# Optimization experiments

Hardware: AMD Instinct MI355X
Metric: run time of the kernel (lower is better)

Reference implementation:

```python
import jax, jax.numpy as jnp
import numpy as np

N_NODES = 100000
N_EDGES = 1600000
D_IN = 64
D_OUT = 64
NEG_SLOPE = 0.2


def setup_inputs() -> dict:
    key = jax.random.key(0)
    ks = jax.random.split(key, 10)
    x = jax.random.normal(ks[0], (N_NODES, D_IN), dtype=jnp.float32)
    edge_index = jax.random.randint(ks[1], (2, N_EDGES), 0, N_NODES, dtype=jnp.int64)
    # glorot-ish scales
    s_lin = 1.0 / np.sqrt(D_IN)
    W_lin = jax.random.normal(ks[2], (D_IN, D_OUT), dtype=jnp.float32) * s_lin
    att_src = jax.random.normal(ks[3], (D_OUT,), dtype=jnp.float32) * s_lin
    att_dst = jax.random.normal(ks[4], (D_OUT,), dtype=jnp.float32) * s_lin
    bias = jnp.zeros((D_OUT,), dtype=jnp.float32)
    W1 = jax.random.normal(ks[5], (D_IN, D_OUT // 2), dtype=jnp.float32) * s_lin
    b1 = jnp.zeros((D_OUT // 2,), dtype=jnp.float32)
    W2 = jax.random.normal(ks[6], (D_OUT // 2, 1), dtype=jnp.float32) * (1.0 / np.sqrt(D_OUT // 2))
    b2 = jnp.zeros((1,), dtype=jnp.float32)
    return {"x": x, "edge_index": edge_index, "W_lin": W_lin, "att_src": att_src,
            "att_dst": att_dst, "bias": bias, "W1": W1, "b1": b1, "W2": W2, "b2": b2}


def reference(x, edge_index, W_lin, att_src, att_dst, bias, W1, b1, W2, b2):
    N = x.shape[0]
    h = x @ W_lin  # [N, D_OUT]
    # peak detector applied to projected features (module requires in==out)
    peak = jax.nn.sigmoid(jax.nn.gelu(h @ W1 + b1, approximate=False) @ W2 + b2)  # [N,1]
    row, col = edge_index[0], edge_index[1]
    # (cat(src,dst) * att).sum(-1) == (h@att_src)[row] + (h@att_dst)[col]
    a_s = h @ att_src  # [N]
    a_d = h @ att_dst  # [N]
    alpha = a_s[row] + a_d[col]  # [E]
    alpha = jnp.where(alpha >= 0, alpha, NEG_SLOPE * alpha)  # leaky_relu
    # segment softmax keyed on row
    m = jax.ops.segment_max(alpha, row, num_segments=N)  # [N]
    e = jnp.exp(alpha - m[row])
    s = jax.ops.segment_sum(e, row, num_segments=N)  # [N]
    alpha = e / s[row]
    # scatter-add weighted source messages back to row (dropout=identity in eval)
    out = jax.ops.segment_sum(h[row] * alpha[:, None], row, num_segments=N)  # [N, D_OUT]
    out = out * (1.0 + peak) + bias
    return out
```

## Files before the change

kernel.cpp:

```cpp
#include <hip/hip_runtime.h>
#include <math.h>

#define D 64
#define DH 32

typedef __attribute__((ext_vector_type(8))) short bf16x8;
typedef __attribute__((ext_vector_type(4))) float f32x4;

static __device__ __forceinline__ unsigned short f2b(float f) {
    unsigned int u = __builtin_bit_cast(unsigned int, f);
    u += 0x7FFFu + ((u >> 16) & 1u);
    return (unsigned short)(u >> 16);
}
static __device__ __forceinline__ unsigned int pack_b2(float a, float b) {
    return (unsigned int)f2b(a) | ((unsigned int)f2b(b) << 16);
}
static __device__ __forceinline__ float gelu_exact(float v) {
    return 0.5f * v * (1.0f + erff(v * 0.70710678118654752f));
}

__global__ void edge_flag_kernel(const int* __restrict__ row,
                                 unsigned char* __restrict__ flag, int E) {
    int i4 = (blockIdx.x * blockDim.x + threadIdx.x) * 4;
    if (i4 + 3 < E) {
        int4 r = *(const int4*)(row + i4);
        flag[r.x] = 1; flag[r.y] = 1; flag[r.z] = 1; flag[r.w] = 1;
    } else if (i4 < E) {
        for (int j = i4; j < E; ++j) flag[row[j]] = 1;
    }
}

__global__ void prep_kernel(const float* __restrict__ Wlin, const float* __restrict__ W1,
                            const float* __restrict__ bias, const float* __restrict__ b1,
                            const float* __restrict__ W2,
                            uint4* __restrict__ flag4, int nflag4,
                            unsigned short* __restrict__ packAW,
                            unsigned short* __restrict__ packAW1, float* __restrict__ packBias,
                            float* __restrict__ packB1, float* __restrict__ packW2)
{
    const int idx = blockIdx.x * blockDim.x + threadIdx.x;
    const int stride = gridDim.x * blockDim.x;
    const uint4 z = {0u, 0u, 0u, 0u};
    for (int i = idx; i < nflag4; i += stride) flag4[i] = z;

    if (blockIdx.x == 0) {
        const int lane = threadIdx.x & 63, part = threadIdx.x >> 6;
        const int q = lane >> 4, m = lane & 15;
#pragma unroll
        for (int fo = 0; fo < 2; ++fo) {
            const int f = part * 2 + fo, nt = f >> 1, ks = f & 1;
#pragma unroll
            for (int j = 0; j < 8; ++j) {
                const int k = 32 * ks + 8 * q + j, n = 16 * nt + m;
                packAW[(f * 64 + lane) * 8 + j] = f2b(Wlin[k * D + n]);
            }
        }
        {
            const int f = part, ntW = f >> 1, ks = f & 1;
#pragma unroll
            for (int j = 0; j < 8; ++j) {
                const int k = 32 * ks + 8 * q + j, n = 16 * ntW + m;
                packAW1[(f * 64 + lane) * 8 + j] = f2b(W1[k * DH + n]);
            }
        }
#pragma unroll
        for (int r = 0; r < 4; ++r)
            packBias[(part * 64 + lane) * 4 + r] = bias[16 * part + 4 * q + r];
        if (part < 2) {
#pragma unroll
            for (int r = 0; r < 4; ++r)
                packB1[(part * 64 + lane) * 4 + r] = b1[16 * part + 4 * q + r];
        } else {
#pragma unroll
            for (int r = 0; r < 4; ++r)
                packW2[((part - 2) * 64 + lane) * 4 + r] = W2[16 * (part - 2) + 4 * q + r];
        }
    }
}

__global__ __launch_bounds__(128) void gat_mfma3(
    const float* __restrict__ x, const unsigned char* __restrict__ flag,
    const unsigned short* __restrict__ packAW, const unsigned short* __restrict__ packAW1,
    const float* __restrict__ packBias, const float* __restrict__ packB1,
    const float* __restrict__ packW2, const float* __restrict__ b2,
    float* __restrict__ out, int N)
{
    __shared__ unsigned short sH[2][64][72];

    const int tid  = threadIdx.x;
    const int wv   = tid >> 6;
    const int lane = tid & 63;
    const int q    = lane >> 4;
    const int m    = lane & 15;
    const int nodeBase = blockIdx.x * 128 + wv * 64;

    int gn[4]; unsigned char fl[4];
#pragma unroll
    for (int mt = 0; mt < 4; ++mt) {
        int g = nodeBase + 16 * mt + m;
        if (g > N - 1) g = N - 1;
        gn[mt] = g;
        fl[mt] = flag[g];
    }
    const float b2s = b2[0];

    float4 u[4][4];
#pragma unroll
    for (int mt = 0; mt < 4; ++mt) {
        const float* px = x + (size_t)gn[mt] * D + 8 * q;
#pragma unroll
        for (int ks = 0; ks < 2; ++ks) {
            u[mt][2 * ks + 0] = *(const float4*)(px + 32 * ks);
            u[mt][2 * ks + 1] = *(const float4*)(px + 32 * ks + 4);
        }
    }

    bf16x8 aw[4][2];
#pragma unroll
    for (int nt = 0; nt < 4; ++nt)
#pragma unroll
        for (int ks = 0; ks < 2; ++ks)
            aw[nt][ks] = ((const bf16x8*)packAW)[(nt * 2 + ks) * 64 + lane];

    bf16x8 bx[4][2];
#pragma unroll
    for (int mt = 0; mt < 4; ++mt)
#pragma unroll
        for (int ks = 0; ks < 2; ++ks) {
            const float4 u0 = u[mt][2 * ks + 0], u1 = u[mt][2 * ks + 1];
            uint4 pk;
            pk.x = pack_b2(u0.x, u0.y); pk.y = pack_b2(u0.z, u0.w);
            pk.z = pack_b2(u1.x, u1.y); pk.w = pack_b2(u1.z, u1.w);
            bx[mt][ks] = __builtin_bit_cast(bf16x8, pk);
        }

    f32x4 accH[4][4];
#pragma unroll
    for (int mt = 0; mt < 4; ++mt)
#pragma unroll
        for (int nt = 0; nt < 4; ++nt)
            accH[mt][nt] = (f32x4){0.f, 0.f, 0.f, 0.f};
#pragma unroll
    for (int ks = 0; ks < 2; ++ks)
#pragma unroll
        for (int mt = 0; mt < 4; ++mt)
#pragma unroll
            for (int nt = 0; nt < 4; ++nt)
                accH[mt][nt] = __builtin_amdgcn_mfma_f32_16x16x32_bf16(
                    aw[nt][ks], bx[mt][ks], accH[mt][nt], 0, 0, 0);

#pragma unroll
    for (int mt = 0; mt < 4; ++mt)
#pragma unroll
        for (int nt = 0; nt < 4; ++nt) {
            uint2 pk;
            pk.x = pack_b2(accH[mt][nt][0], accH[mt][nt][1]);
            pk.y = pack_b2(accH[mt][nt][2], accH[mt][nt][3]);
            *(uint2*)&sH[wv][16 * mt + m][16 * nt + 4 * q] = pk;
        }
    bf16x8 a2[4][2];
#pragma unroll
    for (int mt = 0; mt < 4; ++mt)
#pragma unroll
        for (int ks = 0; ks < 2; ++ks)
            a2[mt][ks] = *(const bf16x8*)&sH[wv][16 * mt + m][32 * ks + 8 * q];

    bf16x8 aw1[2][2];
#pragma unroll
    for (int nt = 0; nt < 2; ++nt)
#pragma unroll
        for (int ks = 0; ks < 2; ++ks)
            aw1[nt][ks] = ((const bf16x8*)packAW1)[(nt * 2 + ks) * 64 + lane];
    const f32x4 b1v0 = ((const f32x4*)packB1)[0 * 64 + lane];
    const f32x4 b1v1 = ((const f32x4*)packB1)[1 * 64 + lane];
    f32x4 acc2[2][4];
#pragma unroll
    for (int mt = 0; mt < 4; ++mt) { acc2[0][mt] = b1v0; acc2[1][mt] = b1v1; }
#pragma unroll
    for (int ks = 0; ks < 2; ++ks)
#pragma unroll
        for (int nt = 0; nt < 2; ++nt)
#pragma unroll
            for (int mt = 0; mt < 4; ++mt)
                acc2[nt][mt] = __builtin_amdgcn_mfma_f32_16x16x32_bf16(
                    aw1[nt][ks], a2[mt][ks], acc2[nt][mt], 0, 0, 0);

    const f32x4 w2v0 = ((const f32x4*)packW2)[0 * 64 + lane];
    const f32x4 w2v1 = ((const f32x4*)packW2)[1 * 64 + lane];
    float scale[4];
#pragma unroll
    for (int mt = 0; mt < 4; ++mt) {
        float pp = 0.f;
#pragma unroll
        for (int r = 0; r < 4; ++r) {
            pp = fmaf(gelu_exact(acc2[0][mt][r]), w2v0[r], pp);
            pp = fmaf(gelu_exact(acc2[1][mt][r]), w2v1[r], pp);
        }
        pp += __shfl_xor(pp, 16);
        pp += __shfl_xor(pp, 32);
        scale[mt] = (fl[mt] != 0) ? (1.f + 1.f / (1.f + expf(-(pp + b2s)))) : 0.f;
    }

    f32x4 biasv[4];
#pragma unroll
    for (int nt = 0; nt < 4; ++nt) biasv[nt] = ((const f32x4*)packBias)[nt * 64 + lane];
#pragma unroll
    for (int mt = 0; mt < 4; ++mt) {
        const int g = nodeBase + 16 * mt + m;
        if (g < N) {
            float* po = out + (size_t)g * D + 4 * q;
#pragma unroll
            for (int nt = 0; nt < 4; ++nt) {
                f32x4 o;
#pragma unroll
                for (int r = 0; r < 4; ++r)
                    o[r] = fmaf(accH[mt][nt][r], scale[mt], biasv[nt][r]);
                *(f32x4*)(po + 16 * nt) = o;
            }
        }
    }
}

extern "C" void kernel_launch(void* const* d_in, const int* in_sizes, int n_in,
                              void* d_out, int out_size, void* d_ws, size_t ws_size,
                              hipStream_t stream) {
    const float* x    = (const float*)d_in[0];
    const int*   eidx = (const int*)d_in[1];
    const float* Wlin = (const float*)d_in[2];
    const float* bias = (const float*)d_in[5];
    const float* W1   = (const float*)d_in[6];
    const float* b1   = (const float*)d_in[7];
    const float* W2   = (const float*)d_in[8];
    const float* b2   = (const float*)d_in[9];
    float* out = (float*)d_out;

    const int N = in_sizes[0] / D;
    const int E = in_sizes[1] / 2;

    char* ws = (char*)d_ws;
    unsigned char* flag = (unsigned char*)ws;
    const int nflag4 = (N + 15) / 16;
    const size_t off = (((size_t)nflag4 * 16) + 255) & ~(size_t)255;
    unsigned short* packAW  = (unsigned short*)(ws + off);
    unsigned short* packAW1 = (unsigned short*)(ws + off + 8192);
    float*          packBias= (float*)(ws + off + 12288);
    float*          packB1  = (float*)(ws + off + 16384);
    float*          packW2  = (float*)(ws + off + 18432);

    prep_kernel<<<128, 256, 0, stream>>>(Wlin, W1, bias, b1, W2,
                                         (uint4*)flag, nflag4,
                                         packAW, packAW1, packBias, packB1, packW2);
    edge_flag_kernel<<<(E / 4 + 255) / 256, 256, 0, stream>>>(eidx, flag, E);
    gat_mfma3<<<(N + 127) / 128, 128, 0, stream>>>(x, flag, packAW, packAW1,
                                                   packBias, packB1, packW2, b2, out, N);
}
```

Baseline: 36.20 us.

## Stage x tiles and packed weights into LDS via direct global-to-LDS loads

The main kernel now gives each wave 32 nodes instead of 64 and uses 256-thread blocks. It loads x rows and all packed weights and biases straight into LDS with global_load_lds, using an XOR swizzle so the later reads avoid bank conflicts, then reuses the same LDS region for the bf16 hidden staging. The edge-flag kernel now reads each flag and only writes it when it is still unset, cutting redundant byte stores. The cost is a block-wide barrier and 52KB of LDS per block, which may limit occupancy.

```diff
diff --git a/kernel.cpp b/kernel.cpp
--- a/kernel.cpp
+++ b/kernel.cpp
@@ -17,6 +17,11 @@
 }
 static __device__ __forceinline__ float gelu_exact(float v) {
     return 0.5f * v * (1.0f + erff(v * 0.70710678118654752f));
+}
+static __device__ __forceinline__ void gload_lds16(void* l, const void* g) {
+    __builtin_amdgcn_global_load_lds(
+        (const __attribute__((address_space(1))) unsigned int*)g,
+        (__attribute__((address_space(3))) unsigned int*)l, 16, 0, 0);
 }
 
 __global__ void edge_flag_kernel(const int* __restrict__ row,
@@ -24,7 +29,10 @@
     int i4 = (blockIdx.x * blockDim.x + threadIdx.x) * 4;
     if (i4 + 3 < E) {
         int4 r = *(const int4*)(row + i4);
-        flag[r.x] = 1; flag[r.y] = 1; flag[r.z] = 1; flag[r.w] = 1;
+        if (!flag[r.x]) flag[r.x] = 1;
+        if (!flag[r.y]) flag[r.y] = 1;
+        if (!flag[r.z]) flag[r.z] = 1;
+        if (!flag[r.w]) flag[r.w] = 1;
     } else if (i4 < E) {
         for (int j = i4; j < E; ++j) flag[row[j]] = 1;
     }
@@ -78,118 +86,129 @@
     }
 }
 
-__global__ __launch_bounds__(128) void gat_mfma3(
+__global__ __launch_bounds__(256) void gat_mfma4(
     const float* __restrict__ x, const unsigned char* __restrict__ flag,
-    const unsigned short* __restrict__ packAW, const unsigned short* __restrict__ packAW1,
-    const float* __restrict__ packBias, const float* __restrict__ packB1,
-    const float* __restrict__ packW2, const float* __restrict__ b2,
+    const float* __restrict__ packbuf, const float* __restrict__ b2,
     float* __restrict__ out, int N)
 {
-    __shared__ unsigned short sH[2][64][72];
+    __shared__ unsigned char lds[53248];
 
     const int tid  = threadIdx.x;
     const int wv   = tid >> 6;
     const int lane = tid & 63;
     const int q    = lane >> 4;
     const int m    = lane & 15;
-    const int nodeBase = blockIdx.x * 128 + wv * 64;
-
-    int gn[4]; unsigned char fl[4];
-#pragma unroll
-    for (int mt = 0; mt < 4; ++mt) {
+    const int nodeBase = blockIdx.x * 128 + wv * 32;
+    const int XB = wv * 8192;
+
+    unsigned char fl[2];
+#pragma unroll
+    for (int mt = 0; mt < 2; ++mt) {
         int g = nodeBase + 16 * mt + m;
         if (g > N - 1) g = N - 1;
-        gn[mt] = g;
         fl[mt] = flag[g];
     }
     const float b2s = b2[0];
 
-    float4 u[4][4];
-#pragma unroll
-    for (int mt = 0; mt < 4; ++mt) {
-        const float* px = x + (size_t)gn[mt] * D + 8 * q;
+#pragma unroll
+    for (int j = 0; j < 8; ++j) {
+        const int r_loc = j * 4 + (lane >> 4);
+        int grow = nodeBase + r_loc;
+        if (grow > N - 1) grow = N - 1;
+        const int c = lane & 15;
+        const float* src = x + (size_t)grow * D + ((c ^ (r_loc & 7)) * 4);
+        gload_lds16(lds + XB + j * 1024, src);
+    }
+#pragma unroll
+    for (int i = 0; i < 5; ++i) {
+        const int ch = wv * 5 + i;
+        gload_lds16(lds + 32768 + ch * 1024, packbuf + ch * 256 + lane * 4);
+    }
+    __syncthreads();
+
+    bf16x8 aw[4][2];
+#pragma unroll
+    for (int nt = 0; nt < 4; ++nt)
+#pragma unroll
+        for (int ks = 0; ks < 2; ++ks)
+            aw[nt][ks] = *(const bf16x8*)(lds + 32768 + (nt * 2 + ks) * 1024 + lane * 16);
+
+    bf16x8 bx[2][2];
+#pragma unroll
+    for (int mt = 0; mt < 2; ++mt) {
+        const int r = 16 * mt + m;
 #pragma unroll
         for (int ks = 0; ks < 2; ++ks) {
-            u[mt][2 * ks + 0] = *(const float4*)(px + 32 * ks);
-            u[mt][2 * ks + 1] = *(const float4*)(px + 32 * ks + 4);
-        }
-    }
-
-    bf16x8 aw[4][2];
-#pragma unroll
-    for (int nt = 0; nt < 4; ++nt)
-#pragma unroll
-        for (int ks = 0; ks < 2; ++ks)
-            aw[nt][ks] = ((const bf16x8*)packAW)[(nt * 2 + ks) * 64 + lane];
-
-    bf16x8 bx[4][2];
-#pragma unroll
-    for (int mt = 0; mt < 4; ++mt)
-#pragma unroll
-        for (int ks = 0; ks < 2; ++ks) {
-            const float4 u0 = u[mt][2 * ks + 0], u1 = u[mt][2 * ks + 1];
+            const int c0 = ks * 8 + q * 2;
+            const uint4 lo = *(const uint4*)(lds + XB + r * 256 + ((c0 ^ (r & 7)) * 16));
+            const uint4 hi = *(const uint4*)(lds + XB + r * 256 + (((c0 + 1) ^ (r & 7)) * 16));
+            const float4 u0 = __builtin_bit_cast(float4, lo);
+            const float4 u1 = __builtin_bit_cast(float4, hi);
             uint4 pk;
             pk.x = pack_b2(u0.x, u0.y); pk.y = pack_b2(u0.z, u0.w);
             pk.z = pack_b2(u1.x, u1.y); pk.w = pack_b2(u1.z, u1.w);
             bx[mt][ks] = __builtin_bit_cast(bf16x8, pk);
         }
-
-    f32x4 accH[4][4];
-#pragma unroll
-    for (int mt = 0; mt < 4; ++mt)
+    }
+
+    f32x4 accH[2][4];
+#pragma unroll
+    for (int mt = 0; mt < 2; ++mt)
 #pragma unroll
         for (int nt = 0; nt < 4; ++nt)
             accH[mt][nt] = (f32x4){0.f, 0.f, 0.f, 0.f};
 #pragma unroll
     for (int ks = 0; ks < 2; ++ks)
 #pragma unroll
-        for (int mt = 0; mt < 4; ++mt)
+        for (int mt = 0; mt < 2; ++mt)
 #pragma unroll
             for (int nt = 0; nt < 4; ++nt)
                 accH[mt][nt] = __builtin_amdgcn_mfma_f32_16x16x32_bf16(
                     aw[nt][ks], bx[mt][ks], accH[mt][nt], 0, 0, 0);
 
-#pragma unroll
-    for (int mt = 0; mt < 4; ++mt)
+    asm volatile("" ::: "memory");
+#pragma unroll
+    for (int mt = 0; mt < 2; ++mt)
 #pragma unroll
         for (int nt = 0; nt < 4; ++nt) {
             uint2 pk;
             pk.x = pack_b2(accH[mt][nt][0], accH[mt][nt][1]);
             pk.y = pack_b2(accH[mt][nt][2], accH[mt][nt][3]);
-            *(uint2*)&sH[wv][16 * mt + m][16 * nt + 4 * q] = pk;
-        }
-    bf16x8 a2[4][2];
-#pragma unroll
-    for (int mt = 0; mt < 4; ++mt)
+            *(uint2*)(lds + XB + (16 * mt + m) * 144 + (16 * nt + 4 * q) * 2) = pk;
+        }
+    asm volatile("" ::: "memory");
+    bf16x8 a2[2][2];
+#pragma unroll
+    for (int mt = 0; mt < 2; ++mt)
 #pragma unroll
         for (int ks = 0; ks < 2; ++ks)
-            a2[mt][ks] = *(const bf16x8*)&sH[wv][16 * mt + m][32 * ks + 8 * q];
+            a2[mt][ks] = *(const bf16x8*)(lds + XB + (16 * mt + m) * 144 + (32 * ks + 8 * q) * 2);
 
     bf16x8 aw1[2][2];
 #pragma unroll
     for (int nt = 0; nt < 2; ++nt)
 #pragma unroll
         for (int ks = 0; ks < 2; ++ks)
-            aw1[nt][ks] = ((const bf16x8*)packAW1)[(nt * 2 + ks) * 64 + lane];
-    const f32x4 b1v0 = ((const f32x4*)packB1)[0 * 64 + lane];
-    const f32x4 b1v1 = ((const f32x4*)packB1)[1 * 64 + lane];
-    f32x4 acc2[2][4];
-#pragma unroll
-    for (int mt = 0; mt < 4; ++mt) { acc2[0][mt] = b1v0; acc2[1][mt] = b1v1; }
+            aw1[nt][ks] = *(const bf16x8*)(lds + 32768 + (8 + nt * 2 + ks) * 1024 + lane * 16);
+    const f32x4 b1v0 = *(const f32x4*)(lds + 32768 + 16 * 1024 + lane * 16);
+    const f32x4 b1v1 = *(const f32x4*)(lds + 32768 + 17 * 1024 + lane * 16);
+    f32x4 acc2[2][2];
+    acc2[0][0] = b1v0; acc2[0][1] = b1v0;
+    acc2[1][0] = b1v1; acc2[1][1] = b1v1;
 #pragma unroll
     for (int ks = 0; ks < 2; ++ks)
 #pragma unroll
         for (int nt = 0; nt < 2; ++nt)
 #pragma unroll
-            for (int mt = 0; mt < 4; ++mt)
+            for (int mt = 0; mt < 2; ++mt)
                 acc2[nt][mt] = __builtin_amdgcn_mfma_f32_16x16x32_bf16(
                     aw1[nt][ks], a2[mt][ks], acc2[nt][mt], 0, 0, 0);
 
-    const f32x4 w2v0 = ((const f32x4*)packW2)[0 * 64 + lane];
-    const f32x4 w2v1 = ((const f32x4*)packW2)[1 * 64 + lane];
-    float scale[4];
-#pragma unroll
-    for (int mt = 0; mt < 4; ++mt) {
+    const f32x4 w2v0 = *(const f32x4*)(lds + 32768 + 18 * 1024 + lane * 16);
+    const f32x4 w2v1 = *(const f32x4*)(lds + 32768 + 19 * 1024 + lane * 16);
+    float scale[2];
+#pragma unroll
+    for (int mt = 0; mt < 2; ++mt) {
         float pp = 0.f;
 #pragma unroll
         for (int r = 0; r < 4; ++r) {
@@ -203,9 +222,10 @@
 
     f32x4 biasv[4];
 #pragma unroll
-    for (int nt = 0; nt < 4; ++nt) biasv[nt] = ((const f32x4*)packBias)[nt * 64 + lane];
-#pragma unroll
-    for (int mt = 0; mt < 4; ++mt) {
+    for (int nt = 0; nt < 4; ++nt)
+        biasv[nt] = *(const f32x4*)(lds + 32768 + (12 + nt) * 1024 + lane * 16);
+#pragma unroll
+    for (int mt = 0; mt < 2; ++mt) {
         const int g = nodeBase + 16 * mt + m;
         if (g < N) {
             float* po = out + (size_t)g * D + 4 * q;
@@ -241,16 +261,16 @@
     unsigned char* flag = (unsigned char*)ws;
     const int nflag4 = (N + 15) / 16;
     const size_t off = (((size_t)nflag4 * 16) + 255) & ~(size_t)255;
-    unsigned short* packAW  = (unsigned short*)(ws + off);
-    unsigned short* packAW1 = (unsigned short*)(ws + off + 8192);
-    float*          packBias= (float*)(ws + off + 12288);
-    float*          packB1  = (float*)(ws + off + 16384);
-    float*          packW2  = (float*)(ws + off + 18432);
+    unsigned short* packAW   = (unsigned short*)(ws + off);
+    unsigned short* packAW1  = (unsigned short*)(ws + off + 8192);
+    float*          packBias = (float*)(ws + off + 12288);
+    float*          packB1   = (float*)(ws + off + 16384);
+    float*          packW2   = (float*)(ws + off + 18432);
+    const float*    packbuf  = (const float*)(ws + off);
 
     prep_kernel<<<128, 256, 0, stream>>>(Wlin, W1, bias, b1, W2,
                                          (uint4*)flag, nflag4,
                                          packAW, packAW1, packBias, packB1, packW2);
     edge_flag_kernel<<<(E / 4 + 255) / 256, 256, 0, stream>>>(eidx, flag, E);
-    gat_mfma3<<<(N + 127) / 128, 128, 0, stream>>>(x, flag, packAW, packAW1,
-                                                   packBias, packB1, packW2, b2, out, N);
-}
+    gat_mfma4<<<(N + 127) / 128, 256, 0, stream>>>(x, flag, packbuf, b2, out, N);
+}
```

Result: slower. 36.94 us (+2.1%).
